# Performance work log

Hardware: AMD Instinct MI355X
Metric: run time of the kernel (lower is better)

Reference implementation:

```python
import jax, jax.numpy as jnp
import numpy as np

D_MODEL = 1024
NUM_HEADS = 16
THETA = 10000.0
B, S = 4, 2048


def setup_inputs() -> dict:
    key = jax.random.key(0)
    ks = jax.random.split(key, 5)
    scale = 1.0 / np.sqrt(D_MODEL)  # keep logits in a sane range
    return {
        "q_proj_weight": jax.random.normal(ks[0], (D_MODEL, D_MODEL), jnp.float32) * scale,
        "k_proj_weight": jax.random.normal(ks[1], (D_MODEL, D_MODEL), jnp.float32) * scale,
        "v_proj_weight": jax.random.normal(ks[2], (D_MODEL, D_MODEL), jnp.float32) * scale,
        "o_proj_weight": jax.random.normal(ks[3], (D_MODEL, D_MODEL), jnp.float32) * scale,
        "in_features": jax.random.normal(ks[4], (B, S, D_MODEL), jnp.float32),
        "token_positions": jnp.arange(S, dtype=jnp.int32),
    }


def _rope(x, cos, sin):
    # interleaved-pair RoPE: pairs are (x[..., 2i], x[..., 2i+1])
    xe = x[..., 0::2]
    xo = x[..., 1::2]
    re = xe * cos - xo * sin
    ro = xe * sin + xo * cos
    return jnp.stack([re, ro], axis=-1).reshape(x.shape)


def reference(q_proj_weight, k_proj_weight, v_proj_weight, o_proj_weight,
              in_features, token_positions):
    Bv, Sv, _ = in_features.shape
    dk = D_MODEL // NUM_HEADS
    half = dk // 2

    q = in_features @ q_proj_weight.T
    k = in_features @ k_proj_weight.T
    v = in_features @ v_proj_weight.T
    # (B, S, D) -> (B, H, S, dk)
    q = q.reshape(Bv, Sv, NUM_HEADS, dk).transpose(0, 2, 1, 3)
    k = k.reshape(Bv, Sv, NUM_HEADS, dk).transpose(0, 2, 1, 3)
    v = v.reshape(Bv, Sv, NUM_HEADS, dk).transpose(0, 2, 1, 3)

    inv_freq = 1.0 / (THETA ** (jnp.arange(half, dtype=jnp.float32) / half))
    freqs = token_positions.astype(jnp.float32)[:, None] * inv_freq[None, :]  # (S, half)
    cos, sin = jnp.cos(freqs), jnp.sin(freqs)  # broadcast over (B, H, S, half)
    q = _rope(q, cos, sin)
    k = _rope(k, cos, sin)

    scores = jnp.einsum('bhqd,bhkd->bhqk', q, k) / np.sqrt(dk).astype(np.float32)
    causal = jnp.tril(jnp.ones((Sv, Sv), dtype=bool))
    scores = jnp.where(causal, scores, -jnp.inf)
    weights = jax.nn.softmax(scores, axis=-1)
    out = jnp.einsum('bhqk,bhkd->bhqd', weights, v)
    out = out.transpose(0, 2, 1, 3).reshape(Bv, Sv, D_MODEL)
    return out @ o_proj_weight.T
```

## Files before the change

### kernel.cpp

```cpp
#include <hip/hip_runtime.h>
#include <stdint.h>
#include <math.h>

#define NH 16
#define DK 64
#define S_LEN 2048
#define BB 4
#define DM 1024
#define M_TOT (BB*S_LEN)
#define KVT 64
#define KPAD 72
#define QB 128

typedef __attribute__((ext_vector_type(8))) short short8;
typedef __attribute__((ext_vector_type(4))) float floatx4;

typedef const __attribute__((address_space(1))) void gas_t;
typedef __attribute__((address_space(3))) void las_t;

__device__ __forceinline__ void glds16(const void* g, void* l){
  __builtin_amdgcn_global_load_lds((gas_t*)g, (las_t*)l, 16, 0, 0);
}

__device__ __forceinline__ unsigned short f2bf(float f){
  unsigned int u = __float_as_uint(f);
  u += 0x7fffu + ((u >> 16) & 1u);
  return (unsigned short)(u >> 16);
}
__device__ __forceinline__ unsigned int pk_bf_trunc(float a, float b){
  return __builtin_amdgcn_perm(__float_as_uint(b), __float_as_uint(a), 0x07060302u);
}
__device__ __forceinline__ float fast_exp2(float x){
  return __builtin_amdgcn_exp2f(x);
}

__global__ void cast_kernel(const float* __restrict__ in, unsigned short* __restrict__ out, int n){
  int i = (blockIdx.x * blockDim.x + threadIdx.x) * 4;
  if (i < n){
    float4 v = *(const float4*)(in + i);
    ushort4 u;
    u.x = f2bf(v.x); u.y = f2bf(v.y); u.z = f2bf(v.z); u.w = f2bf(v.w);
    *(ushort4*)(out + i) = u;
  }
}

__global__ __launch_bounds__(256) void gemm_qkv(
    const unsigned short* __restrict__ Xb,
    const unsigned short* __restrict__ Wq,
    const unsigned short* __restrict__ Wk,
    const unsigned short* __restrict__ Wv,
    const int* __restrict__ pos,
    unsigned short* __restrict__ Qo,
    unsigned short* __restrict__ Ko,
    unsigned short* __restrict__ VTo)
{
  const int K = DM;
  __shared__ __align__(16) unsigned short As[128 * 32];
  __shared__ __align__(16) unsigned short Bs[128 * 32];
  int m0 = blockIdx.x * 128;
  int n0 = blockIdx.y * 128;
  int z  = blockIdx.z;
  const unsigned short* Bmat = (z == 0) ? Wq : ((z == 1) ? Wk : Wv);
  unsigned short* Out = (z == 0) ? Qo : ((z == 1) ? Ko : VTo);

  int tid = threadIdx.x;
  int wave = tid >> 6, lane = tid & 63;
  int l15 = lane & 15, quad = lane >> 4;
  int wm = (wave >> 1) * 64, wn = (wave & 1) * 64;

  floatx4 acc[4][4] = {};

  for (int k0 = 0; k0 < K; k0 += 32){
    #pragma unroll
    for (int j = 0; j < 2; j++){
      int c = j * 256 + tid;
      int row = c >> 2, seg = c & 3;
      glds16(&Xb[(size_t)(m0 + row) * K + k0 + seg * 8],   (char*)As + (size_t)c * 16);
      glds16(&Bmat[(size_t)(n0 + row) * K + k0 + seg * 8], (char*)Bs + (size_t)c * 16);
    }
    __syncthreads();
    short8 a[4], b[4];
    #pragma unroll
    for (int mi = 0; mi < 4; mi++) a[mi] = *(const short8*)&As[(wm + mi * 16 + l15) * 32 + quad * 8];
    #pragma unroll
    for (int ni = 0; ni < 4; ni++) b[ni] = *(const short8*)&Bs[(wn + ni * 16 + l15) * 32 + quad * 8];
    #pragma unroll
    for (int mi = 0; mi < 4; mi++)
      #pragma unroll
      for (int ni = 0; ni < 4; ni++)
        acc[mi][ni] = __builtin_amdgcn_mfma_f32_16x16x32_bf16(a[mi], b[ni], acc[mi][ni], 0, 0, 0);
    __syncthreads();
  }

  if (z == 2){
    #pragma unroll
    for (int mi = 0; mi < 4; mi++){
      int row0 = m0 + wm + mi * 16 + quad * 4;
      int bb2 = row0 >> 11, s0 = row0 & (S_LEN - 1);
      #pragma unroll
      for (int ni = 0; ni < 4; ni++){
        int col = n0 + wn + ni * 16 + l15;
        int h = col >> 6, d = col & 63;
        ushort4 u;
        u.x = f2bf(acc[mi][ni][0]); u.y = f2bf(acc[mi][ni][1]);
        u.z = f2bf(acc[mi][ni][2]); u.w = f2bf(acc[mi][ni][3]);
        *(ushort4*)&Out[(((size_t)bb2 * NH + h) * DK + d) * S_LEN + s0] = u;
      }
    }
  } else {
    const float SC = (z == 0) ? 0.180336879f : 1.0f;
    #pragma unroll
    for (int mi = 0; mi < 4; mi++){
      #pragma unroll
      for (int ni = 0; ni < 4; ni++){
        int col = n0 + wn + ni * 16 + l15;
        int h = col >> 6, d = col & 63;
        int fi = d >> 1, odd = d & 1;
        float invfrev = fast_exp2(-(float)fi * (13.2877123795494f / 32.0f)) * 0.15915494309f;
        #pragma unroll
        for (int r = 0; r < 4; r++){
          int row = m0 + wm + mi * 16 + quad * 4 + r;
          int bb2 = row >> 11, s = row & (S_LEN - 1);
          float p = (float)pos[s];
          float rev = p * invfrev;
          rev = rev - floorf(rev);
          float c  = __builtin_amdgcn_cosf(rev);
          float sn = __builtin_amdgcn_sinf(rev);
          float val = acc[mi][ni][r];
          float other = __shfl_xor(val, 1);
          float outv = odd ? (other * sn + val * c) : (val * c - other * sn);
          Out[(((size_t)bb2 * NH + h) * S_LEN + s) * DK + d] = f2bf(outv * SC);
        }
      }
    }
  }
}

__global__ __launch_bounds__(256) void gemm_out(
    const unsigned short* __restrict__ Ab,
    const unsigned short* __restrict__ Wo,
    float* __restrict__ Out)
{
  const int K = DM;
  __shared__ __align__(16) unsigned short As[128 * 32];
  __shared__ __align__(16) unsigned short Bs[128 * 32];
  int m0 = blockIdx.x * 128;
  int n0 = blockIdx.y * 128;

  int tid = threadIdx.x;
  int wave = tid >> 6, lane = tid & 63;
  int l15 = lane & 15, quad = lane >> 4;
  int wm = (wave >> 1) * 64, wn = (wave & 1) * 64;

  floatx4 acc[4][4] = {};

  for (int k0 = 0; k0 < K; k0 += 32){
    #pragma unroll
    for (int j = 0; j < 2; j++){
      int c = j * 256 + tid;
      int row = c >> 2, seg = c & 3;
      glds16(&Ab[(size_t)(m0 + row) * K + k0 + seg * 8], (char*)As + (size_t)c * 16);
      glds16(&Wo[(size_t)(n0 + row) * K + k0 + seg * 8], (char*)Bs + (size_t)c * 16);
    }
    __syncthreads();
    short8 a[4], b[4];
    #pragma unroll
    for (int mi = 0; mi < 4; mi++) a[mi] = *(const short8*)&As[(wm + mi * 16 + l15) * 32 + quad * 8];
    #pragma unroll
    for (int ni = 0; ni < 4; ni++) b[ni] = *(const short8*)&Bs[(wn + ni * 16 + l15) * 32 + quad * 8];
    #pragma unroll
    for (int mi = 0; mi < 4; mi++)
      #pragma unroll
      for (int ni = 0; ni < 4; ni++)
        acc[mi][ni] = __builtin_amdgcn_mfma_f32_16x16x32_bf16(a[mi], b[ni], acc[mi][ni], 0, 0, 0);
    __syncthreads();
  }

  #pragma unroll
  for (int mi = 0; mi < 4; mi++){
    #pragma unroll
    for (int ni = 0; ni < 4; ni++){
      #pragma unroll
      for (int r = 0; r < 4; r++){
        int row = m0 + wm + mi * 16 + quad * 4 + r;
        int col = n0 + wn + ni * 16 + l15;
        Out[(size_t)row * DM + col] = acc[mi][ni][r];
      }
    }
  }
}

__global__ __launch_bounds__(256) void attn_kernel(
    const unsigned short* __restrict__ Qg,
    const unsigned short* __restrict__ Kg,
    const unsigned short* __restrict__ VTg,
    unsigned short* __restrict__ Ao)
{
  __shared__ __align__(16) unsigned short Ks[KVT * KPAD];
  __shared__ __align__(16) unsigned short Vs[DK * KPAD];
  __shared__ __align__(16) unsigned short Ps[4][32 * KPAD];

  int bh = blockIdx.x;
  int q0 = ((int)gridDim.y - 1 - (int)blockIdx.y) * QB;
  int tid = threadIdx.x, wave = tid >> 6, lane = tid & 63;
  int l15 = lane & 15, quad = lane >> 4;
  int qw = q0 + wave * 32;

  const unsigned short* Qb = Qg + (size_t)bh * S_LEN * DK;
  const unsigned short* Kb = Kg + (size_t)bh * S_LEN * DK;
  const unsigned short* Vb = VTg + (size_t)bh * DK * S_LEN;

  short8 aq[2][2];
  #pragma unroll
  for (int mi = 0; mi < 2; mi++){
    aq[mi][0] = *(const short8*)&Qb[(qw + mi * 16 + l15) * DK + quad * 8];
    aq[mi][1] = *(const short8*)&Qb[(qw + mi * 16 + l15) * DK + 32 + quad * 8];
  }

  floatx4 o[2][4] = {};
  float lsum[2][4] = {{0.f,0.f,0.f,0.f},{0.f,0.f,0.f,0.f}};

  int srow = tid >> 2;
  int scol = (tid & 3) * 16;
  int kpos = (srow & 3) * 16 + (srow >> 2);
  const unsigned short* Krow = Kb + (size_t)srow * DK + scol;
  const unsigned short* Vrow = Vb + (size_t)srow * S_LEN + scol;
  unsigned short* KsW = &Ks[kpos * KPAD + scol];
  unsigned short* VsW = &Vs[srow * KPAD + scol];

  int nt = q0 / KVT + 2;

  short8 kr0 = *(const short8*)(Krow);
  short8 kr1 = *(const short8*)(Krow + 8);
  short8 vr0 = *(const short8*)(Vrow);
  short8 vr1 = *(const short8*)(Vrow + 8);

  for (int kt = 0; kt < nt; kt++){
    int kv0 = kt * KVT;
    __syncthreads();
    *(short8*)(KsW)     = kr0;
    *(short8*)(KsW + 8) = kr1;
    *(short8*)(VsW)     = vr0;
    *(short8*)(VsW + 8) = vr1;
    if (kt + 1 < nt){
      int kvn = kv0 + KVT;
      kr0 = *(const short8*)(Krow + (size_t)kvn * DK);
      kr1 = *(const short8*)(Krow + (size_t)kvn * DK + 8);
      vr0 = *(const short8*)(Vrow + kvn);
      vr1 = *(const short8*)(Vrow + kvn + 8);
    }
    __syncthreads();

    if (kv0 <= qw + 31){
      floatx4 sc[2][4] = {};
      #pragma unroll
      for (int ni = 0; ni < 4; ni++){
        short8 bk0 = *(const short8*)&Ks[(ni * 16 + l15) * KPAD + quad * 8];
        short8 bk1 = *(const short8*)&Ks[(ni * 16 + l15) * KPAD + 32 + quad * 8];
        #pragma unroll
        for (int mi = 0; mi < 2; mi++){
          sc[mi][ni] = __builtin_amdgcn_mfma_f32_16x16x32_bf16(aq[mi][0], bk0, sc[mi][ni], 0, 0, 0);
          sc[mi][ni] = __builtin_amdgcn_mfma_f32_16x16x32_bf16(aq[mi][1], bk1, sc[mi][ni], 0, 0, 0);
        }
      }
      bool full = (kv0 + 63 <= qw);
      int kvb = kv0 + 4 * l15;
      #pragma unroll
      for (int mi = 0; mi < 2; mi++){
        #pragma unroll
        for (int r = 0; r < 4; r++){
          int qg = qw + mi * 16 + quad * 4 + r;
          float v0 = sc[mi][0][r], v1 = sc[mi][1][r], v2 = sc[mi][2][r], v3 = sc[mi][3][r];
          if (!full){
            v0 = (kvb     > qg) ? -INFINITY : v0;
            v1 = (kvb + 1 > qg) ? -INFINITY : v1;
            v2 = (kvb + 2 > qg) ? -INFINITY : v2;
            v3 = (kvb + 3 > qg) ? -INFINITY : v3;
          }
          float p0 = fast_exp2(v0);
          float p1 = fast_exp2(v1);
          float p2 = fast_exp2(v2);
          float p3 = fast_exp2(v3);
          lsum[mi][r] += (p0 + p1) + (p2 + p3);
          uint2 u;
          u.x = pk_bf_trunc(p0, p1);
          u.y = pk_bf_trunc(p2, p3);
          *(uint2*)&Ps[wave][(mi * 16 + quad * 4 + r) * KPAD + 4 * l15] = u;
        }
      }
      asm volatile("s_waitcnt lgkmcnt(0)" ::: "memory");
      short8 ap[2][2];
      #pragma unroll
      for (int mi = 0; mi < 2; mi++){
        ap[mi][0] = *(const short8*)&Ps[wave][(mi * 16 + l15) * KPAD + quad * 8];
        ap[mi][1] = *(const short8*)&Ps[wave][(mi * 16 + l15) * KPAD + 32 + quad * 8];
      }
      #pragma unroll
      for (int dt = 0; dt < 4; dt++){
        short8 bv0 = *(const short8*)&Vs[(dt * 16 + l15) * KPAD + quad * 8];
        short8 bv1 = *(const short8*)&Vs[(dt * 16 + l15) * KPAD + 32 + quad * 8];
        #pragma unroll
        for (int mi = 0; mi < 2; mi++){
          o[mi][dt] = __builtin_amdgcn_mfma_f32_16x16x32_bf16(ap[mi][0], bv0, o[mi][dt], 0, 0, 0);
          o[mi][dt] = __builtin_amdgcn_mfma_f32_16x16x32_bf16(ap[mi][1], bv1, o[mi][dt], 0, 0, 0);
        }
      }
    }
  }

  float linv[2][4];
  #pragma unroll
  for (int mi = 0; mi < 2; mi++){
    #pragma unroll
    for (int r = 0; r < 4; r++){
      float rs = lsum[mi][r];
      rs += __shfl_xor(rs, 1);
      rs += __shfl_xor(rs, 2);
      rs += __shfl_xor(rs, 4);
      rs += __shfl_xor(rs, 8);
      linv[mi][r] = 1.0f / rs;
    }
  }

  int bq = bh >> 4, hq = bh & 15;
  #pragma unroll
  for (int mi = 0; mi < 2; mi++){
    #pragma unroll
    for (int dt = 0; dt < 4; dt++){
      #pragma unroll
      for (int r = 0; r < 4; r++){
        float val = o[mi][dt][r] * linv[mi][r];
        int s = qw + mi * 16 + quad * 4 + r;
        int d = dt * 16 + l15;
        Ao[(((size_t)bq * S_LEN + s) * NH + hq) * DK + d] = f2bf(val);
      }
    }
  }
}

extern "C" void kernel_launch(void* const* d_in, const int* in_sizes, int n_in,
                              void* d_out, int out_size, void* d_ws, size_t ws_size,
                              hipStream_t stream) {
  (void)in_sizes; (void)n_in; (void)out_size; (void)ws_size;
  const float* Wq = (const float*)d_in[0];
  const float* Wk = (const float*)d_in[1];
  const float* Wv = (const float*)d_in[2];
  const float* Wo = (const float*)d_in[3];
  const float* X  = (const float*)d_in[4];
  const int* pos  = (const int*)d_in[5];
  float* out = (float*)d_out;

  char* ws = (char*)d_ws;
  const size_t MB = 1024 * 1024;
  unsigned short* Xb  = (unsigned short*)(ws);
  unsigned short* Wqb = (unsigned short*)(ws + 16 * MB);
  unsigned short* Wkb = (unsigned short*)(ws + 18 * MB);
  unsigned short* Wvb = (unsigned short*)(ws + 20 * MB);
  unsigned short* Wob = (unsigned short*)(ws + 22 * MB);
  unsigned short* Qb  = (unsigned short*)(ws + 24 * MB);
  unsigned short* Kb  = (unsigned short*)(ws + 40 * MB);
  unsigned short* Vb  = (unsigned short*)(ws + 56 * MB);
  unsigned short* Ab  = (unsigned short*)(ws + 72 * MB);

  cast_kernel<<<8192, 256, 0, stream>>>(X,  Xb,  M_TOT * DM);
  cast_kernel<<<1024, 256, 0, stream>>>(Wq, Wqb, DM * DM);
  cast_kernel<<<1024, 256, 0, stream>>>(Wk, Wkb, DM * DM);
  cast_kernel<<<1024, 256, 0, stream>>>(Wv, Wvb, DM * DM);
  cast_kernel<<<1024, 256, 0, stream>>>(Wo, Wob, DM * DM);

  gemm_qkv<<<dim3(64, 8, 3), 256, 0, stream>>>(Xb, Wqb, Wkb, Wvb, pos, Qb, Kb, Vb);
  attn_kernel<<<dim3(64, S_LEN / QB), 256, 0, stream>>>(Qb, Kb, Vb, Ab);
  gemm_out<<<dim3(64, 8), 256, 0, stream>>>(Ab, Wob, out);
}
```

Measured before the change: 264.1 us.

## Triple-buffer GEMM tiles with XOR-swizzled LDS and larger 256x128 blocks

Replaces the single-buffered 128x128x32 GEMM loop in the QKV and output projections with a shared core that uses 256x128 tiles, BK=64, 512 threads and a three-stage global-to-LDS pipeline with explicit vmcnt waits and one barrier per iteration. LDS rows are XOR-swizzled to avoid bank conflicts, and MFMA sections are wrapped in setprio. The aim is to hide global load latency behind MFMA work and raise data reuse per block. In exchange it uses much more LDS (about 144KB), which with launch_bounds(512,2) may limit occupancy, and it halves the number of blocks.

```diff
diff --git a/kernel.cpp b/kernel.cpp
--- a/kernel.cpp
+++ b/kernel.cpp
@@ -12,6 +12,13 @@
 #define KPAD 72
 #define QB 128
 
+#define BM 256
+#define BN 128
+#define BK 64
+#define NTK (DM/BK)
+#define LDS_A_BUF (BM*BK)
+#define LDS_B_BUF (BN*BK)
+
 typedef __attribute__((ext_vector_type(8))) short short8;
 typedef __attribute__((ext_vector_type(4))) float floatx4;
 
@@ -44,7 +51,82 @@
   }
 }
 
-__global__ __launch_bounds__(256) void gemm_qkv(
+__device__ __forceinline__ void stage_tile(const unsigned short* __restrict__ A,
+                                           const unsigned short* __restrict__ Bm,
+                                           int m0, int n0, int k0,
+                                           unsigned short* As, unsigned short* Bs, int tid)
+{
+  #pragma unroll
+  for (int j = 0; j < 4; j++){
+    int c = j*512 + tid;
+    int r = c >> 3;
+    int sl = (c & 7) ^ (r & 7);
+    glds16(&A[(size_t)(m0 + r)*DM + k0 + sl*8], (char*)As + (size_t)c*16);
+  }
+  #pragma unroll
+  for (int j = 0; j < 2; j++){
+    int c = j*512 + tid;
+    int r = c >> 3;
+    int sl = (c & 7) ^ (r & 7);
+    glds16(&Bm[(size_t)(n0 + r)*DM + k0 + sl*8], (char*)Bs + (size_t)c*16);
+  }
+}
+
+__device__ __forceinline__ void gemm_core(const unsigned short* __restrict__ A,
+                                          const unsigned short* __restrict__ Bm,
+                                          int m0, int n0, unsigned short* Ls,
+                                          int tid, floatx4 (&acc)[4][4])
+{
+  unsigned short* AsB = Ls;
+  unsigned short* BsB = Ls + 3*LDS_A_BUF;
+  int wave = tid >> 6, lane = tid & 63;
+  int l15 = lane & 15, quad = lane >> 4;
+  int wm = (wave >> 1) * 64, wn = (wave & 1) * 64;
+  int s0 = quad ^ (l15 & 7);
+
+  stage_tile(A, Bm, m0, n0, 0,  AsB,             BsB,             tid);
+  stage_tile(A, Bm, m0, n0, BK, AsB + LDS_A_BUF, BsB + LDS_B_BUF, tid);
+  asm volatile("s_waitcnt vmcnt(6)" ::: "memory");
+  __builtin_amdgcn_s_barrier();
+
+  #pragma unroll
+  for (int t = 0; t < NTK; ++t){
+    const int bufc = t % 3;
+    if (t + 2 < NTK){
+      const int bn = (t + 2) % 3;
+      stage_tile(A, Bm, m0, n0, (t+2)*BK, AsB + bn*LDS_A_BUF, BsB + bn*LDS_B_BUF, tid);
+    }
+    const unsigned short* Ab = AsB + bufc*LDS_A_BUF;
+    const unsigned short* Bb = BsB + bufc*LDS_B_BUF;
+    short8 a[4][2], b[4][2];
+    #pragma unroll
+    for (int mi = 0; mi < 4; mi++){
+      const unsigned short* pr = Ab + (wm + mi*16 + l15)*BK;
+      a[mi][0] = *(const short8*)(pr + s0*8);
+      a[mi][1] = *(const short8*)(pr + (s0^4)*8);
+    }
+    #pragma unroll
+    for (int ni = 0; ni < 4; ni++){
+      const unsigned short* pr = Bb + (wn + ni*16 + l15)*BK;
+      b[ni][0] = *(const short8*)(pr + s0*8);
+      b[ni][1] = *(const short8*)(pr + (s0^4)*8);
+    }
+    __builtin_amdgcn_s_setprio(1);
+    #pragma unroll
+    for (int mi = 0; mi < 4; mi++)
+      #pragma unroll
+      for (int ni = 0; ni < 4; ni++){
+        acc[mi][ni] = __builtin_amdgcn_mfma_f32_16x16x32_bf16(a[mi][0], b[ni][0], acc[mi][ni], 0, 0, 0);
+        acc[mi][ni] = __builtin_amdgcn_mfma_f32_16x16x32_bf16(a[mi][1], b[ni][1], acc[mi][ni], 0, 0, 0);
+      }
+    __builtin_amdgcn_s_setprio(0);
+    if (t + 2 < NTK)      { asm volatile("s_waitcnt vmcnt(6)" ::: "memory"); }
+    else if (t + 1 < NTK) { asm volatile("s_waitcnt vmcnt(0)" ::: "memory"); }
+    if (t + 1 < NTK) __builtin_amdgcn_s_barrier();
+  }
+}
+
+__global__ __launch_bounds__(512, 2) void gemm_qkv(
     const unsigned short* __restrict__ Xb,
     const unsigned short* __restrict__ Wq,
     const unsigned short* __restrict__ Wk,
@@ -54,49 +136,26 @@
     unsigned short* __restrict__ Ko,
     unsigned short* __restrict__ VTo)
 {
-  const int K = DM;
-  __shared__ __align__(16) unsigned short As[128 * 32];
-  __shared__ __align__(16) unsigned short Bs[128 * 32];
-  int m0 = blockIdx.x * 128;
-  int n0 = blockIdx.y * 128;
+  __shared__ __align__(16) unsigned short Ls[3*LDS_A_BUF + 3*LDS_B_BUF];
+  int m0 = blockIdx.x * BM;
+  int n0 = blockIdx.y * BN;
   int z  = blockIdx.z;
   const unsigned short* Bmat = (z == 0) ? Wq : ((z == 1) ? Wk : Wv);
   unsigned short* Out = (z == 0) ? Qo : ((z == 1) ? Ko : VTo);
 
   int tid = threadIdx.x;
+  floatx4 acc[4][4] = {};
+  gemm_core(Xb, Bmat, m0, n0, Ls, tid, acc);
+
   int wave = tid >> 6, lane = tid & 63;
   int l15 = lane & 15, quad = lane >> 4;
   int wm = (wave >> 1) * 64, wn = (wave & 1) * 64;
 
-  floatx4 acc[4][4] = {};
-
-  for (int k0 = 0; k0 < K; k0 += 32){
-    #pragma unroll
-    for (int j = 0; j < 2; j++){
-      int c = j * 256 + tid;
-      int row = c >> 2, seg = c & 3;
-      glds16(&Xb[(size_t)(m0 + row) * K + k0 + seg * 8],   (char*)As + (size_t)c * 16);
-      glds16(&Bmat[(size_t)(n0 + row) * K + k0 + seg * 8], (char*)Bs + (size_t)c * 16);
-    }
-    __syncthreads();
-    short8 a[4], b[4];
-    #pragma unroll
-    for (int mi = 0; mi < 4; mi++) a[mi] = *(const short8*)&As[(wm + mi * 16 + l15) * 32 + quad * 8];
-    #pragma unroll
-    for (int ni = 0; ni < 4; ni++) b[ni] = *(const short8*)&Bs[(wn + ni * 16 + l15) * 32 + quad * 8];
-    #pragma unroll
-    for (int mi = 0; mi < 4; mi++)
-      #pragma unroll
-      for (int ni = 0; ni < 4; ni++)
-        acc[mi][ni] = __builtin_amdgcn_mfma_f32_16x16x32_bf16(a[mi], b[ni], acc[mi][ni], 0, 0, 0);
-    __syncthreads();
-  }
-
   if (z == 2){
     #pragma unroll
     for (int mi = 0; mi < 4; mi++){
       int row0 = m0 + wm + mi * 16 + quad * 4;
-      int bb2 = row0 >> 11, s0 = row0 & (S_LEN - 1);
+      int bb2 = row0 >> 11, sQ = row0 & (S_LEN - 1);
       #pragma unroll
       for (int ni = 0; ni < 4; ni++){
         int col = n0 + wn + ni * 16 + l15;
@@ -104,7 +163,7 @@
         ushort4 u;
         u.x = f2bf(acc[mi][ni][0]); u.y = f2bf(acc[mi][ni][1]);
         u.z = f2bf(acc[mi][ni][2]); u.w = f2bf(acc[mi][ni][3]);
-        *(ushort4*)&Out[(((size_t)bb2 * NH + h) * DK + d) * S_LEN + s0] = u;
+        *(ushort4*)&Out[(((size_t)bb2 * NH + h) * DK + d) * S_LEN + sQ] = u;
       }
     }
   } else {
@@ -136,45 +195,22 @@
   }
 }
 
-__global__ __launch_bounds__(256) void gemm_out(
+__global__ __launch_bounds__(512, 2) void gemm_out(
     const unsigned short* __restrict__ Ab,
     const unsigned short* __restrict__ Wo,
     float* __restrict__ Out)
 {
-  const int K = DM;
-  __shared__ __align__(16) unsigned short As[128 * 32];
-  __shared__ __align__(16) unsigned short Bs[128 * 32];
-  int m0 = blockIdx.x * 128;
-  int n0 = blockIdx.y * 128;
+  __shared__ __align__(16) unsigned short Ls[3*LDS_A_BUF + 3*LDS_B_BUF];
+  int m0 = blockIdx.x * BM;
+  int n0 = blockIdx.y * BN;
 
   int tid = threadIdx.x;
+  floatx4 acc[4][4] = {};
+  gemm_core(Ab, Wo, m0, n0, Ls, tid, acc);
+
   int wave = tid >> 6, lane = tid & 63;
   int l15 = lane & 15, quad = lane >> 4;
   int wm = (wave >> 1) * 64, wn = (wave & 1) * 64;
-
-  floatx4 acc[4][4] = {};
-
-  for (int k0 = 0; k0 < K; k0 += 32){
-    #pragma unroll
-    for (int j = 0; j < 2; j++){
-      int c = j * 256 + tid;
-      int row = c >> 2, seg = c & 3;
-      glds16(&Ab[(size_t)(m0 + row) * K + k0 + seg * 8], (char*)As + (size_t)c * 16);
-      glds16(&Wo[(size_t)(n0 + row) * K + k0 + seg * 8], (char*)Bs + (size_t)c * 16);
-    }
-    __syncthreads();
-    short8 a[4], b[4];
-    #pragma unroll
-    for (int mi = 0; mi < 4; mi++) a[mi] = *(const short8*)&As[(wm + mi * 16 + l15) * 32 + quad * 8];
-    #pragma unroll
-    for (int ni = 0; ni < 4; ni++) b[ni] = *(const short8*)&Bs[(wn + ni * 16 + l15) * 32 + quad * 8];
-    #pragma unroll
-    for (int mi = 0; mi < 4; mi++)
-      #pragma unroll
-      for (int ni = 0; ni < 4; ni++)
-        acc[mi][ni] = __builtin_amdgcn_mfma_f32_16x16x32_bf16(a[mi], b[ni], acc[mi][ni], 0, 0, 0);
-    __syncthreads();
-  }
 
   #pragma unroll
   for (int mi = 0; mi < 4; mi++){
@@ -368,7 +404,7 @@
   cast_kernel<<<1024, 256, 0, stream>>>(Wv, Wvb, DM * DM);
   cast_kernel<<<1024, 256, 0, stream>>>(Wo, Wob, DM * DM);
 
-  gemm_qkv<<<dim3(64, 8, 3), 256, 0, stream>>>(Xb, Wqb, Wkb, Wvb, pos, Qb, Kb, Vb);
+  gemm_qkv<<<dim3(M_TOT/BM, DM/BN, 3), 512, 0, stream>>>(Xb, Wqb, Wkb, Wvb, pos, Qb, Kb, Vb);
   attn_kernel<<<dim3(64, S_LEN / QB), 256, 0, stream>>>(Qb, Kb, Vb, Ab);
-  gemm_out<<<dim3(64, 8), 256, 0, stream>>>(Ab, Wob, out);
-}
+  gemm_out<<<dim3(M_TOT/BM, DM/BN), 512, 0, stream>>>(Ab, Wob, out);
+}
```

New measurement: 234.7 us. -11.2%, faster.
